# Kernel tuning notes

Hardware: AMD Instinct MI355X
Metric: run time of the kernel (lower is better)

## Reference

```python
import jax, jax.numpy as jnp
import numpy as np

H = 256
B = 32768
ADV, GOOD, BOX, RAMP = 8, 8, 16, 8
OTHER = ADV + GOOD - 1
OBS = 10 + 10 * OTHER + 13 * BOX + 12 * RAMP  # 464


def _lin(k, din, dout):
    return jax.random.normal(k, (din, dout), dtype=jnp.float32) * (1.0 / np.sqrt(din))


def setup_inputs() -> dict:
    key = jax.random.key(0)
    ks = jax.random.split(key, 12)
    return {
        "inputs": jax.random.normal(ks[0], (B, OBS), dtype=jnp.float32),
        "W_self": _lin(ks[1], 10, H), "b_self": jnp.zeros((H,), jnp.float32),
        "W_other": _lin(ks[2], 10, H), "b_other": jnp.zeros((H,), jnp.float32),
        "W_box": _lin(ks[3], 13, H), "b_box": jnp.zeros((H,), jnp.float32),
        "W_ramp": _lin(ks[4], 12, H), "b_ramp": jnp.zeros((H,), jnp.float32),
        "corr_other": _lin(ks[5], H, H),
        "corr_box": _lin(ks[6], H, H),
        "corr_ramp": _lin(ks[7], H, H),
        "W_fc": _lin(ks[8], H, H), "b_fc": jnp.zeros((H,), jnp.float32),
        "W_e1": _lin(ks[9], 4 * H, H), "b_e1": jnp.zeros((H,), jnp.float32),
        "W_e2": _lin(ks[10], H, H), "b_e2": jnp.zeros((H,), jnp.float32),
        "adv_num": ADV, "good_num": GOOD, "box_num": BOX, "ramp_num": RAMP,
        "agent_i": 0,
    }


def _attend_pool(emb_self, corr, ents, W, b):
    # ents: [B, N, F] raw entity features -> encode, bilinear score vs self, softmax, pool
    emb = jnp.tanh(jnp.einsum('bnf,fh->bnh', ents, W) + b)        # [B,N,H]
    beta = jnp.einsum('bh,hk,bnk->bn', emb_self, corr, emb)        # [B,N]
    alpha = jax.nn.softmax(beta, axis=1)                           # [B,N]
    return jnp.einsum('bn,bnh->bh', alpha, emb)                    # [B,H]


def reference(inputs, W_self, b_self, W_other, b_other, W_box, b_box,
              W_ramp, b_ramp, corr_other, corr_box, corr_ramp,
              W_fc, b_fc, W_e1, b_e1, W_e2, b_e2,
              adv_num, good_num, box_num, ramp_num, agent_i):
    bsz = inputs.shape[0]
    other_nums = adv_num + good_num - 1
    o0 = 10
    o1 = o0 + 10 * other_nums
    o2 = o1 + 13 * box_num
    o3 = o2 + 12 * ramp_num

    self_in = inputs[:, :o0]                                   # [B,10]
    other_in = inputs[:, o0:o1].reshape(bsz, other_nums, 10)   # [B,N_o,10]
    box_in = inputs[:, o1:o2].reshape(bsz, box_num, 13)        # [B,N_b,13]
    ramp_in = inputs[:, o2:o3].reshape(bsz, ramp_num, 12)      # [B,N_r,12]

    emb_self = jnp.tanh(self_in @ W_self + b_self)             # [B,H]

    vi_other = _attend_pool(emb_self, corr_other, other_in, W_other, b_other)
    vi_box = _attend_pool(emb_self, corr_box, box_in, W_box, b_box)
    vi_ramp = _attend_pool(emb_self, corr_ramp, ramp_in, W_ramp, b_ramp)

    gi = jnp.tanh(emb_self @ W_fc + b_fc)                      # [B,H]
    cat = jnp.concatenate([gi, vi_other, vi_box, vi_ramp], axis=1)  # [B,4H]
    h = jnp.tanh(cat @ W_e1 + b_e1)
    return jnp.tanh(h @ W_e2 + b_e2)                           # [B,H]
```

## Files before the change

kernel.cpp:

```cpp
#include <hip/hip_runtime.h>
#include <hip/hip_bf16.h>

#define HDIM   256
#define OBS    464
#define MROWS  16
#define NW     8

#define OFF_FC 196608
#define OFF_E1 262144
#define OFF_E2 524288
#define TOTW   589824

typedef __attribute__((ext_vector_type(8))) short short8;
typedef __attribute__((ext_vector_type(4))) float f32x4;
typedef unsigned short u16;

__device__ __forceinline__ float fast_tanh(float x) {
    float e = __expf(2.0f * x);
    return 1.0f - 2.0f * __builtin_amdgcn_rcpf(e + 1.0f);
}

template <bool BF16>
__device__ __forceinline__ float loadf(const void* p, int i) {
    if constexpr (BF16)
        return __bfloat162float(((const __hip_bfloat16*)p)[i]);
    else
        return ((const float*)p)[i];
}

__device__ __forceinline__ u16 f2bf(float x) {
    __hip_bfloat16 b = __float2bfloat16(x);
    return *reinterpret_cast<u16*>(&b);
}

__device__ __forceinline__ float b2f(u16 u) {
    return __uint_as_float(((unsigned)u) << 16);
}

__device__ __forceinline__ void split1(float v, u16& hi, u16& lo) {
    unsigned u = __float_as_uint(v);
    hi = (u16)(u >> 16);
    lo = f2bf(v - __uint_as_float(u & 0xffff0000u));
}

__device__ __forceinline__ f32x4 mfma3(short8 ah, short8 al, short8 bh, short8 bl, f32x4 c) {
    c = __builtin_amdgcn_mfma_f32_16x16x32_bf16(ah, bh, c, 0, 0, 0);
    c = __builtin_amdgcn_mfma_f32_16x16x32_bf16(al, bh, c, 0, 0, 0);
    c = __builtin_amdgcn_mfma_f32_16x16x32_bf16(ah, bl, c, 0, 0, 0);
    return c;
}

template <int CTRL>
__device__ __forceinline__ float dpp_ror_add(float p) {
    int r = __builtin_amdgcn_update_dpp(0, __float_as_int(p), CTRL, 0xf, 0xf, false);
    return p + __int_as_float(r);
}

__device__ __forceinline__ float wave_sum(float p) {
    p = dpp_ror_add<0x121>(p);
    p = dpp_ror_add<0x122>(p);
    p = dpp_ror_add<0x124>(p);
    p = dpp_ror_add<0x128>(p);
    p += __shfl_xor(p, 16, 64);
    p += __shfl_xor(p, 32, 64);
    return p;
}

__device__ __forceinline__ int pidx(int row, int col) {
    return row * HDIM + (col ^ ((row & 7) << 3));
}

__device__ __forceinline__ void store_act(u16* __restrict__ hiP, u16* __restrict__ loP,
                                          int row, int col, float v) {
    u16 h, s;
    split1(v, h, s);
    const int i = pidx(row, col);
    hiP[i] = h;
    loP[i] = s;
}

__device__ __forceinline__ void lda_p(const u16* __restrict__ hiP, const u16* __restrict__ loP,
                                      int l, int kbase, short8& ah, short8& al) {
    const int row = l & 15;
    const int col = kbase + ((l >> 4) << 3);
    const int idx = row * HDIM + (col ^ ((row & 7) << 3));
    ah = *(const short8*)(hiP + idx);
    al = *(const short8*)(loP + idx);
}

__device__ __forceinline__ void mm2(const u16* __restrict__ hiP, const u16* __restrict__ loP,
                                    const u16* __restrict__ Whi, const u16* __restrict__ Wlo,
                                    int seg, int ks0, int wv, int l, f32x4 acc[2]) {
#pragma unroll 2
    for (int ks = 0; ks < 8; ++ks) {
        short8 ah, al;
        lda_p(hiP, loP, l, ks << 5, ah, al);
        const u16* bp = Whi + seg + ((ks0 + ks) << 13) + (l << 3);
        const u16* lp = Wlo + seg + ((ks0 + ks) << 13) + (l << 3);
#pragma unroll
        for (int c4 = 0; c4 < 2; ++c4) {
            const int ct = (wv << 1) + c4;
            short8 bh = *(const short8*)(bp + (ct << 9));
            short8 bl = *(const short8*)(lp + (ct << 9));
            acc[c4] = mfma3(ah, al, bh, bl, acc[c4]);
        }
    }
}

template <bool BF16, int N, int F, int BASE>
__device__ __forceinline__ void attend_group(int wv, int l, const void* __restrict__ x,
                                             int rb, int Bn,
                                             u16* __restrict__ hiP, u16* __restrict__ loP,
                                             const void* __restrict__ W,
                                             const void* __restrict__ b) {
    float wreg[F][4];
#pragma unroll
    for (int k = 0; k < F; ++k)
#pragma unroll
        for (int c = 0; c < 4; ++c)
            wreg[k][c] = loadf<BF16>(W, k * HDIM + c * 64 + l);
    const float b0 = loadf<BF16>(b, l);
    const float b1 = loadf<BF16>(b, 64 + l);
    const float b2 = loadf<BF16>(b, 128 + l);
    const float b3 = loadf<BF16>(b, 192 + l);
#pragma unroll 1
    for (int t = 0; t < 2; ++t) {
        const int r = (wv << 1) + t;
        int row = rb + r; if (row >= Bn) row = Bn - 1;
        const unsigned urow = (unsigned)__builtin_amdgcn_readfirstlane(row);
        const unsigned* xd = (const unsigned*)x + ((urow * OBS + BASE) >> 1);
        const float*    xf = (const float*)x + (urow * OBS + BASE);
        const int i0 = pidx(r, l), i1 = pidx(r, 64 + l), i2 = pidx(r, 128 + l), i3 = pidx(r, 192 + l);
        const float q0 = b2f(hiP[i0]) + b2f(loP[i0]);
        const float q1 = b2f(hiP[i1]) + b2f(loP[i1]);
        const float q2 = b2f(hiP[i2]) + b2f(loP[i2]);
        const float q3 = b2f(hiP[i3]) + b2f(loP[i3]);
        float s = 0.0f;
        float v0 = 0.f, v1 = 0.f, v2 = 0.f, v3 = 0.f;
#pragma unroll 4
        for (int n = 0; n < N; ++n) {
            float a0 = b0, a1 = b1, a2 = b2, a3 = b3;
#pragma unroll
            for (int k = 0; k < F; ++k) {
                const int jj = n * F + k;
                float xv;
                if constexpr (BF16) {
                    unsigned d = xd[jj >> 1];
                    xv = __uint_as_float((jj & 1) ? (d & 0xffff0000u) : (d << 16));
                } else {
                    xv = xf[jj];
                }
                a0 = fmaf(xv, wreg[k][0], a0);
                a1 = fmaf(xv, wreg[k][1], a1);
                a2 = fmaf(xv, wreg[k][2], a2);
                a3 = fmaf(xv, wreg[k][3], a3);
            }
            float e0 = fast_tanh(a0), e1 = fast_tanh(a1);
            float e2 = fast_tanh(a2), e3 = fast_tanh(a3);
            float p = q0 * e0;
            p = fmaf(q1, e1, p);
            p = fmaf(q2, e2, p);
            p = fmaf(q3, e3, p);
            p = wave_sum(p);
            float w = __expf(p);
            s += w;
            v0 = fmaf(w, e0, v0);
            v1 = fmaf(w, e1, v1);
            v2 = fmaf(w, e2, v2);
            v3 = fmaf(w, e3, v3);
        }
        float inv = __builtin_amdgcn_rcpf(s);
        store_act(hiP, loP, r, l,       v0 * inv);
        store_act(hiP, loP, r, 64 + l,  v1 * inv);
        store_act(hiP, loP, r, 128 + l, v2 * inv);
        store_act(hiP, loP, r, 192 + l, v3 * inv);
    }
}

__global__ void dtype_probe(const unsigned short* __restrict__ x, int* __restrict__ flag) {
    if (threadIdx.x == 0 && blockIdx.x == 0) {
        int cnt = 0;
        for (int i = 0; i < 256; ++i) {
            unsigned short u = x[2 * i];
            int e = (u >> 7) & 0xFF;
            if (e >= 118 && e <= 132) cnt++;
        }
        *flag = (cnt >= 128) ? 1 : 0;
    }
}

template <bool BF16>
__global__ void prep_weights(const void* __restrict__ c0, const void* __restrict__ c1,
                             const void* __restrict__ c2, const void* __restrict__ fc,
                             const void* __restrict__ e1, const void* __restrict__ e2,
                             u16* __restrict__ Whi, u16* __restrict__ Wlo,
                             const int* __restrict__ flag) {
    if (*flag != (BF16 ? 1 : 0)) return;
    int idx = blockIdx.x * 256 + threadIdx.x;
    if (idx >= TOTW) return;
    const void* src;
    int base;
    if (idx < OFF_FC)      { int m = idx >> 16; src = (m == 0) ? c0 : ((m == 1) ? c1 : c2); base = m << 16; }
    else if (idx < OFF_E1) { src = fc; base = OFF_FC; }
    else if (idx < OFF_E2) { src = e1; base = OFF_E1; }
    else                   { src = e2; base = OFF_E2; }
    int local = idx - base;
    int i  = local & 7;
    int ln = (local >> 3) & 63;
    int ct = (local >> 9) & 15;
    int ks = local >> 13;
    int k = (ks << 5) + ((ln >> 4) << 3) + i;
    int c = (ct << 4) + (ln & 15);
    float v = loadf<BF16>(src, k * HDIM + c);
    u16 h, s;
    split1(v, h, s);
    Whi[idx] = h;
    Wlo[idx] = s;
}

template <bool BF16>
__global__ __launch_bounds__(512, 4) void obs_mfma(
    const void* __restrict__ inputs,
    const void* __restrict__ W_self, const void* __restrict__ b_self,
    const void* __restrict__ W_other, const void* __restrict__ b_other,
    const void* __restrict__ W_box, const void* __restrict__ b_box,
    const void* __restrict__ W_ramp, const void* __restrict__ b_ramp,
    const void* __restrict__ b_fc, const void* __restrict__ b_e1,
    const void* __restrict__ b_e2,
    const u16* __restrict__ Whi, const u16* __restrict__ Wlo,
    void* __restrict__ out, const int* __restrict__ flag, int Bn) {
    if (*flag != (BF16 ? 1 : 0)) return;

    __shared__ u16 sAh[MROWS * HDIM], sAl[MROWS * HDIM];
    __shared__ u16 sBh[MROWS * HDIM], sBl[MROWS * HDIM];

    const int tid = threadIdx.x;
    const int rb = blockIdx.x * MROWS;
    const int wv = tid >> 6, l = tid & 63;
    const f32x4 z = {0.f, 0.f, 0.f, 0.f};

    {
        const int col = tid & 255, rh = tid >> 8;
        float acc[8];
        float bv = loadf<BF16>(b_self, col);
#pragma unroll
        for (int r = 0; r < 8; ++r) acc[r] = bv;
#pragma unroll
        for (int k = 0; k < 10; ++k) {
            float w = loadf<BF16>(W_self, k * HDIM + col);
#pragma unroll
            for (int r = 0; r < 8; ++r) {
                int row = rb + rh * 8 + r; if (row >= Bn) row = Bn - 1;
                acc[r] = fmaf(loadf<BF16>(inputs, row * OBS + k), w, acc[r]);
            }
        }
#pragma unroll
        for (int r = 0; r < 8; ++r)
            store_act(sAh, sAl, rh * 8 + r, col, fast_tanh(acc[r]));
    }
    __syncthreads();

    {
        f32x4 acc[2] = {z, z};
        mm2(sAh, sAl, Whi, Wlo, OFF_FC, 0, wv, l, acc);
#pragma unroll
        for (int c4 = 0; c4 < 2; ++c4) {
            const int ct = (wv << 1) + c4, col = (ct << 4) + (l & 15);
            float bv = loadf<BF16>(b_fc, col);
#pragma unroll
            for (int i = 0; i < 4; ++i) {
                const int row = ((l >> 4) << 2) + i;
                store_act(sBh, sBl, row, col, fast_tanh(acc[c4][i] + bv));
            }
        }
    }
    __syncthreads();

    f32x4 accE1[2] = {z, z};
    mm2(sBh, sBl, Whi, Wlo, OFF_E1, 0, wv, l, accE1);
    __syncthreads();

#pragma unroll
    for (int g = 0; g < 3; ++g) {
        {
            f32x4 acc[2] = {z, z};
            mm2(sAh, sAl, Whi, Wlo, g << 16, 0, wv, l, acc);
#pragma unroll
            for (int c4 = 0; c4 < 2; ++c4) {
                const int ct = (wv << 1) + c4, col = (ct << 4) + (l & 15);
#pragma unroll
                for (int i = 0; i < 4; ++i) {
                    const int row = ((l >> 4) << 2) + i;
                    store_act(sBh, sBl, row, col, acc[c4][i]);
                }
            }
        }
        __syncthreads();
        if (g == 0)      attend_group<BF16, 15, 10,  10>(wv, l, inputs, rb, Bn, sBh, sBl, W_other, b_other);
        else if (g == 1) attend_group<BF16, 16, 13, 160>(wv, l, inputs, rb, Bn, sBh, sBl, W_box,  b_box);
        else             attend_group<BF16,  8, 12, 368>(wv, l, inputs, rb, Bn, sBh, sBl, W_ramp, b_ramp);
        __syncthreads();
        mm2(sBh, sBl, Whi, Wlo, OFF_E1, (g + 1) << 3, wv, l, accE1);
        __syncthreads();
    }

#pragma unroll
    for (int c4 = 0; c4 < 2; ++c4) {
        const int ct = (wv << 1) + c4, col = (ct << 4) + (l & 15);
        float bv = loadf<BF16>(b_e1, col);
#pragma unroll
        for (int i = 0; i < 4; ++i) {
            const int row = ((l >> 4) << 2) + i;
            store_act(sAh, sAl, row, col, fast_tanh(accE1[c4][i] + bv));
        }
    }
    __syncthreads();

    {
        f32x4 acc[2] = {z, z};
        mm2(sAh, sAl, Whi, Wlo, OFF_E2, 0, wv, l, acc);
#pragma unroll
        for (int c4 = 0; c4 < 2; ++c4) {
            const int ct = (wv << 1) + c4, col = (ct << 4) + (l & 15);
            float bv = loadf<BF16>(b_e2, col);
#pragma unroll
            for (int i = 0; i < 4; ++i) {
                const int row = rb + ((l >> 4) << 2) + i;
                if (row < Bn) {
                    float v = fast_tanh(acc[c4][i] + bv);
                    if constexpr (BF16)
                        ((__hip_bfloat16*)out)[row * HDIM + col] = __float2bfloat16(v);
                    else
                        ((float*)out)[row * HDIM + col] = v;
                }
            }
        }
    }
}

extern "C" void kernel_launch(void* const* d_in, const int* in_sizes, int n_in,
                              void* d_out, int out_size, void* d_ws, size_t ws_size,
                              hipStream_t stream) {
    const int Bn = in_sizes[0] / OBS;
    int* flag = (int*)d_ws;
    u16* Whi = (u16*)((char*)d_ws + 256);
    u16* Wlo = Whi + TOTW;

    dtype_probe<<<1, 64, 0, stream>>>((const unsigned short*)d_in[0], flag);

    const int pgrid = (TOTW + 255) / 256;
    prep_weights<true><<<pgrid, 256, 0, stream>>>(
        d_in[9], d_in[10], d_in[11], d_in[12], d_in[14], d_in[16], Whi, Wlo, flag);
    prep_weights<false><<<pgrid, 256, 0, stream>>>(
        d_in[9], d_in[10], d_in[11], d_in[12], d_in[14], d_in[16], Whi, Wlo, flag);

    const int grid = (Bn + MROWS - 1) / MROWS;
    obs_mfma<true><<<grid, 512, 0, stream>>>(
        d_in[0], d_in[1], d_in[2], d_in[3], d_in[4], d_in[5], d_in[6], d_in[7],
        d_in[8], d_in[13], d_in[15], d_in[17], Whi, Wlo, d_out, flag, Bn);
    obs_mfma<false><<<grid, 512, 0, stream>>>(
        d_in[0], d_in[1], d_in[2], d_in[3], d_in[4], d_in[5], d_in[6], d_in[7],
        d_in[8], d_in[13], d_in[15], d_in[17], Whi, Wlo, d_out, flag, Bn);
}
```

Before: 514.0 us.

## Double-buffer attention query tiles to interleave stages and drop barriers

Adds a second shared-memory buffer for the per-group query/pooled tiles. The three attention groups are now software-pipelined: the next group's query matmul and the previous group's E1 accumulation run in the same phase as the current group's attention pooling. This removes several __syncthreads and gives the scheduler independent MFMA and VALU work to mix. In exchange, shared memory per block rises by one more buffer pair, and launch bounds drop from 4 to 2 blocks per CU, which allows more registers but may reduce occupancy.

```diff
diff --git a/kernel.cpp b/kernel.cpp
--- a/kernel.cpp
+++ b/kernel.cpp
@@ -103,6 +103,19 @@
             short8 bh = *(const short8*)(bp + (ct << 9));
             short8 bl = *(const short8*)(lp + (ct << 9));
             acc[c4] = mfma3(ah, al, bh, bl, acc[c4]);
+        }
+    }
+}
+
+__device__ __forceinline__ void store_q(const f32x4 acc[2], u16* __restrict__ hiP,
+                                        u16* __restrict__ loP, int wv, int l) {
+#pragma unroll
+    for (int c4 = 0; c4 < 2; ++c4) {
+        const int ct = (wv << 1) + c4, col = (ct << 4) + (l & 15);
+#pragma unroll
+        for (int i = 0; i < 4; ++i) {
+            const int row = ((l >> 4) << 2) + i;
+            store_act(hiP, loP, row, col, acc[c4][i]);
         }
     }
 }
@@ -219,7 +232,7 @@
 }
 
 template <bool BF16>
-__global__ __launch_bounds__(512, 4) void obs_mfma(
+__global__ __launch_bounds__(512, 2) void obs_mfma(
     const void* __restrict__ inputs,
     const void* __restrict__ W_self, const void* __restrict__ b_self,
     const void* __restrict__ W_other, const void* __restrict__ b_other,
@@ -232,7 +245,8 @@
     if (*flag != (BF16 ? 1 : 0)) return;
 
     __shared__ u16 sAh[MROWS * HDIM], sAl[MROWS * HDIM];
-    __shared__ u16 sBh[MROWS * HDIM], sBl[MROWS * HDIM];
+    __shared__ u16 sB0h[MROWS * HDIM], sB0l[MROWS * HDIM];
+    __shared__ u16 sB1h[MROWS * HDIM], sB1l[MROWS * HDIM];
 
     const int tid = threadIdx.x;
     const int rb = blockIdx.x * MROWS;
@@ -270,40 +284,45 @@
 #pragma unroll
             for (int i = 0; i < 4; ++i) {
                 const int row = ((l >> 4) << 2) + i;
-                store_act(sBh, sBl, row, col, fast_tanh(acc[c4][i] + bv));
+                store_act(sB0h, sB0l, row, col, fast_tanh(acc[c4][i] + bv));
             }
         }
     }
     __syncthreads();
 
     f32x4 accE1[2] = {z, z};
-    mm2(sBh, sBl, Whi, Wlo, OFF_E1, 0, wv, l, accE1);
-    __syncthreads();
-
-#pragma unroll
-    for (int g = 0; g < 3; ++g) {
-        {
-            f32x4 acc[2] = {z, z};
-            mm2(sAh, sAl, Whi, Wlo, g << 16, 0, wv, l, acc);
-#pragma unroll
-            for (int c4 = 0; c4 < 2; ++c4) {
-                const int ct = (wv << 1) + c4, col = (ct << 4) + (l & 15);
-#pragma unroll
-                for (int i = 0; i < 4; ++i) {
-                    const int row = ((l >> 4) << 2) + i;
-                    store_act(sBh, sBl, row, col, acc[c4][i]);
-                }
-            }
-        }
-        __syncthreads();
-        if (g == 0)      attend_group<BF16, 15, 10,  10>(wv, l, inputs, rb, Bn, sBh, sBl, W_other, b_other);
-        else if (g == 1) attend_group<BF16, 16, 13, 160>(wv, l, inputs, rb, Bn, sBh, sBl, W_box,  b_box);
-        else             attend_group<BF16,  8, 12, 368>(wv, l, inputs, rb, Bn, sBh, sBl, W_ramp, b_ramp);
-        __syncthreads();
-        mm2(sBh, sBl, Whi, Wlo, OFF_E1, (g + 1) << 3, wv, l, accE1);
-        __syncthreads();
-    }
-
+    mm2(sB0h, sB0l, Whi, Wlo, OFF_E1, 0, wv, l, accE1);
+    {
+        f32x4 accq[2] = {z, z};
+        mm2(sAh, sAl, Whi, Wlo, 0 << 16, 0, wv, l, accq);
+        store_q(accq, sB1h, sB1l, wv, l);
+    }
+    __syncthreads();
+
+    {
+        f32x4 accq[2] = {z, z};
+        mm2(sAh, sAl, Whi, Wlo, 1 << 16, 0, wv, l, accq);
+        attend_group<BF16, 15, 10, 10>(wv, l, inputs, rb, Bn, sB1h, sB1l, W_other, b_other);
+        store_q(accq, sB0h, sB0l, wv, l);
+    }
+    __syncthreads();
+
+    mm2(sB1h, sB1l, Whi, Wlo, OFF_E1, 8, wv, l, accE1);
+    attend_group<BF16, 16, 13, 160>(wv, l, inputs, rb, Bn, sB0h, sB0l, W_box, b_box);
+    __syncthreads();
+
+    mm2(sB0h, sB0l, Whi, Wlo, OFF_E1, 16, wv, l, accE1);
+    {
+        f32x4 accq[2] = {z, z};
+        mm2(sAh, sAl, Whi, Wlo, 2 << 16, 0, wv, l, accq);
+        store_q(accq, sB1h, sB1l, wv, l);
+    }
+    __syncthreads();
+
+    attend_group<BF16, 8, 12, 368>(wv, l, inputs, rb, Bn, sB1h, sB1l, W_ramp, b_ramp);
+    __syncthreads();
+
+    mm2(sB1h, sB1l, Whi, Wlo, OFF_E1, 24, wv, l, accE1);
 #pragma unroll
     for (int c4 = 0; c4 < 2; ++c4) {
         const int ct = (wv << 1) + c4, col = (ct << 4) + (l & 15);
```

New measurement: 707.1 us. +37.6%, slower.
